# Performance work log

Hardware: AMD Instinct MI355X
Metric: run time of the kernel (lower is better)

## Reference

```python
import jax, jax.numpy as jnp
import numpy as np

EPS = 1e-5
SLOPE = 0.2
K = 20
B, N = 8, 2048

def _lrelu(x):
    return jnp.where(x >= 0, x, SLOPE * x)

def _bn(x, g, b, m, v, axis):
    # eval-mode batchnorm with running stats
    shape = [1] * x.ndim
    shape[axis] = -1
    g, b, m, v = (t.reshape(shape) for t in (g, b, m, v))
    return g * (x - m) * jax.lax.rsqrt(v + EPS) + b

def _knn(x, k):
    # x: (B, C, N) -> neighbor indices (B, N, k) by largest negative sq dist
    xx = jnp.sum(x * x, axis=1)                      # (B, N)
    inner = jnp.einsum('bcn,bcm->bnm', x, x)         # (B, N, N)
    pd = 2.0 * inner - xx[:, :, None] - xx[:, None, :]
    return jax.lax.top_k(pd, k)[1]

def _graph_feature(x, k):
    # x: (B, C, N) -> (B, 2C, N, k) edge features [nbr - center, center]
    idx = _knn(x, k)                                  # (B, N, k)
    xt = jnp.transpose(x, (0, 2, 1))                  # (B, N, C)
    nbr = xt[jnp.arange(x.shape[0])[:, None, None], idx]  # (B, N, k, C)
    center = xt[:, :, None, :]
    f = jnp.concatenate([nbr - center, jnp.broadcast_to(center, nbr.shape)], axis=-1)
    return jnp.transpose(f, (0, 3, 1, 2))

def _edge_block(x, W, g, b, m, v):
    f = _graph_feature(x, K)                          # (B, 2C, N, k)
    h = jnp.einsum('oc,bcnk->bonk', W, f)             # 1x1 conv
    return jnp.max(_lrelu(_bn(h, g, b, m, v, 1)), axis=-1)

def _forward(x, W1, bn1_g, bn1_b, bn1_m, bn1_v, W2, bn2_g, bn2_b, bn2_m, bn2_v, W3, bn3_g, bn3_b, bn3_m, bn3_v, W4, bn4_g, bn4_b, bn4_m, bn4_v, l1_w, l1_b, bn5_g, bn5_b, bn5_m, bn5_v, l2_w, l2_b, bn6_g, bn6_b, bn6_m, bn6_v, l3_w, l3_b):
    xc = jnp.transpose(x, (0, 2, 1))                  # (B, 3, N)
    x1 = _edge_block(xc, W1, bn1_g, bn1_b, bn1_m, bn1_v)   # (B, 64, N)
    x2 = _edge_block(x1, W2, bn2_g, bn2_b, bn2_m, bn2_v)   # (B, 64, N)
    x3 = _edge_block(x2, W3, bn3_g, bn3_b, bn3_m, bn3_v)   # (B, 128, N)
    h = jnp.concatenate([x1, x2, x3], axis=1)         # (B, 256, N)
    h = _lrelu(_bn(jnp.einsum('oc,bcn->bon', W4, h), bn4_g, bn4_b, bn4_m, bn4_v, 1))
    h = jnp.max(h, axis=-1)                           # (B, 1024)
    h = _lrelu(_bn(h @ l1_w.T + l1_b, bn5_g, bn5_b, bn5_m, bn5_v, 1))
    h = _lrelu(_bn(h @ l2_w.T + l2_b, bn6_g, bn6_b, bn6_m, bn6_v, 1))
    return h @ l3_w.T + l3_b                          # (B, 2)

def setup_inputs() -> dict:
    key = jax.random.key(0)
    ks = iter(jax.random.split(key, 64))
    def rn(shape, s=1.0):
        return jax.random.normal(next(ks), shape, jnp.float32) * s
    def add_bn(inp, prefix, c):
        inp[prefix + '_g'] = jax.random.uniform(next(ks), (c,), jnp.float32, 0.5, 1.5)
        inp[prefix + '_b'] = rn((c,), 0.1)
        inp[prefix + '_m'] = rn((c,), 0.1)
        inp[prefix + '_v'] = jax.random.uniform(next(ks), (c,), jnp.float32, 0.5, 1.5)
    inp = {'x': rn((B, N, 3))}
    inp['W1'] = rn((64, 6), 0.3); add_bn(inp, 'bn1', 64)
    inp['W2'] = rn((64, 128), 0.1); add_bn(inp, 'bn2', 64)
    inp['W3'] = rn((128, 128), 0.1); add_bn(inp, 'bn3', 128)
    inp['W4'] = rn((1024, 256), 0.08); add_bn(inp, 'bn4', 1024)
    inp['l1_w'] = rn((512, 1024), 0.03); inp['l1_b'] = rn((512,), 0.01); add_bn(inp, 'bn5', 512)
    inp['l2_w'] = rn((256, 512), 0.05); inp['l2_b'] = rn((256,), 0.01); add_bn(inp, 'bn6', 256)
    inp['l3_w'] = rn((2, 256), 0.06); inp['l3_b'] = rn((2,), 0.01)
    return inp

def reference(x, W1, bn1_g, bn1_b, bn1_m, bn1_v, W2, bn2_g, bn2_b, bn2_m, bn2_v, W3, bn3_g, bn3_b, bn3_m, bn3_v, W4, bn4_g, bn4_b, bn4_m, bn4_v, l1_w, l1_b, bn5_g, bn5_b, bn5_m, bn5_v, l2_w, l2_b, bn6_g, bn6_b, bn6_m, bn6_v, l3_w, l3_b):
    return _forward(x, W1, bn1_g, bn1_b, bn1_m, bn1_v, W2, bn2_g, bn2_b, bn2_m, bn2_v, W3, bn3_g, bn3_b, bn3_m, bn3_v, W4, bn4_g, bn4_b, bn4_m, bn4_v, l1_w, l1_b, bn5_g, bn5_b, bn5_m, bn5_v, l2_w, l2_b, bn6_g, bn6_b, bn6_m, bn6_v, l3_w, l3_b)
```

## Files before the change

kernel.cpp:

```cpp
#include <hip/hip_runtime.h>
#include <math.h>

#define BB 8
#define NN 2048
#define KK 20
#define EPSF 1e-5f
#define QB 32
#define NSP 8

__device__ __forceinline__ float lrelu(float v){ return v >= 0.f ? v : 0.2f*v; }

__device__ __forceinline__ void topk20_insert(float d, int idc, float (&v)[KK], int (&id)[KK]){
#pragma unroll
  for (int j = KK-1; j >= 1; --j){
    bool cjm1 = d > v[j-1];
    bool cj   = d > v[j];
    float nv = cjm1 ? v[j-1] : (cj ? d   : v[j]);
    int   ni = cjm1 ? id[j-1] : (cj ? idc : id[j]);
    v[j] = nv; id[j] = ni;
  }
  if (d > v[0]) { v[0] = d; id[0] = idc; }
}

__global__ void k_prep1(const float* __restrict__ x, const float* __restrict__ W1,
                        float* __restrict__ Y, float* __restrict__ T, float* __restrict__ SQ){
  __shared__ float wa[64][3], wd[64][3];
  int t = threadIdx.x;
  if (t < 64){
#pragma unroll
    for (int c=0;c<3;c++){
      float a = W1[t*6+c], b2 = W1[t*6+3+c];
      wa[t][c] = a; wd[t][c] = b2 - a;
    }
  }
  __syncthreads();
  int gid = blockIdx.x*256 + t;
  int b = gid >> 11, n = gid & (NN-1);
  float px = x[gid*3+0], py = x[gid*3+1], pz = x[gid*3+2];
  SQ[gid] = px*px + py*py + pz*pz;
  float* yb = Y + ((size_t)b*128)*NN + n;
  float* tb = T + ((size_t)b*128)*NN + n;
#pragma unroll 8
  for (int o=0;o<64;o++){
    yb[(size_t)o*NN] = wa[o][0]*px + wa[o][1]*py + wa[o][2]*pz;
    tb[(size_t)o*NN] = wd[o][0]*px + wd[o][1]*py + wd[o][2]*pz;
  }
}

__global__ __launch_bounds__(256) void k_knn3(const float* __restrict__ x, const float* __restrict__ SQ,
                                              int* __restrict__ IDX){
  __shared__ __align__(16) unsigned char smem[40960];
  float* cd = (float*)smem;
  float* VL = (float*)smem;
  int*   IL = (int*)(smem + 20480);
  int t = threadIdx.x;
  int b = blockIdx.x >> 6;
  int n_base = (blockIdx.x & 63) * QB;
  int ql = t & 31, sp = t >> 5;
  int n = n_base + ql;
  int gq = b*NN + n;
  float qx = x[gq*3], qy = x[gq*3+1], qz = x[gq*3+2];
  float qs = SQ[gq];
  float v[KK]; int id[KK];
#pragma unroll
  for (int i=0;i<KK;i++){ v[i] = -INFINITY; id[i] = 0; }
  int mlo = sp * 16;
  for (int tile=0; tile<16; ++tile){
    int m0 = tile * 128;
    __syncthreads();
#pragma unroll
    for (int i=0;i<2;i++){
      int f2 = t + i*256;
      int m = f2 >> 2, ch = f2 & 3;
      int gm = b*NN + m0 + m;
      cd[f2] = (ch < 3) ? x[gm*3 + ch] : SQ[gm];
    }
    __syncthreads();
    for (int j=mlo; j<mlo+16; ++j){
      float4 c4 = *(const float4*)&cd[j*4];
      float d = 2.f*(qx*c4.x + qy*c4.y + qz*c4.z) - qs - c4.w;
      if (d > v[KK-1]) topk20_insert(d, m0 + j, v, id);
    }
  }
  __syncthreads();
#pragma unroll
  for (int k2=0;k2<KK;k2++){
    VL[(ql*NSP+sp)*KK + k2] = v[k2];
    IL[(ql*NSP+sp)*KK + k2] = id[k2];
  }
  __syncthreads();
  if (t < QB){
    float hv[NSP]; int hi_[NSP]; int hp[NSP];
#pragma unroll
    for (int s=0;s<NSP;s++){ hp[s]=0; hv[s]=VL[(t*NSP+s)*KK]; hi_[s]=IL[(t*NSP+s)*KK]; }
    int nq = n_base + t;
    for (int r=0;r<KK;r++){
      float bv = hv[0]; int bi = hi_[0]; int bs = 0;
#pragma unroll
      for (int s=1;s<NSP;s++){
        bool win = (hv[s] > bv) || ((hv[s] == bv) && (hi_[s] < bi));
        bv = win ? hv[s] : bv; bi = win ? hi_[s] : bi; bs = win ? s : bs;
      }
      IDX[((size_t)b*KK + r)*NN + nq] = bi;
#pragma unroll
      for (int s=0;s<NSP;s++){
        if (s == bs){
          int np = hp[s] + 1; hp[s] = np;
          bool ok = np < KK;
          hv[s]  = ok ? VL[(t*NSP+s)*KK + np] : -INFINITY;
          hi_[s] = ok ? IL[(t*NSP+s)*KK + np] : 0x7FFFFFFF;
        }
      }
    }
  }
}

__global__ __launch_bounds__(256) void k_knn64(const float* __restrict__ X, const float* __restrict__ SQ,
                                               int* __restrict__ IDX){
  __shared__ __align__(16) unsigned char smem[40960];
  float* cd = (float*)smem;
  float* cs = (float*)(smem + 34816);
  float* VL = (float*)smem;
  int*   IL = (int*)(smem + 20480);
  int t = threadIdx.x;
  int b = blockIdx.x >> 6;
  int n_base = (blockIdx.x & 63) * QB;
  int ql = t & 31, sp = t >> 5;
  int n = n_base + ql;
  const float* xb = X + (size_t)b*256*NN;
  float q[64];
#pragma unroll
  for (int c=0;c<64;c++) q[c] = xb[(size_t)c*NN + n];
  float qs = SQ[b*NN + n];
  float v[KK]; int id[KK];
#pragma unroll
  for (int i=0;i<KK;i++){ v[i]=-INFINITY; id[i]=0; }
  int mlo = sp * 16;
  for (int tile=0; tile<16; ++tile){
    int m0 = tile*128;
    __syncthreads();
#pragma unroll
    for (int i=0;i<32;i++){
      int flat = i*256 + t;
      int c = flat >> 7, m = flat & 127;
      cd[m*68 + c] = xb[(size_t)c*NN + m0 + m];
    }
    if (t < 128) cs[t] = SQ[b*NN + m0 + t];
    __syncthreads();
    for (int j=mlo; j<mlo+16; ++j){
      float d = 0.f;
#pragma unroll
      for (int c=0;c<64;c+=4){
        float4 c4 = *(const float4*)&cd[j*68 + c];
        d += q[c]*c4.x + q[c+1]*c4.y + q[c+2]*c4.z + q[c+3]*c4.w;
      }
      d = 2.f*d - qs - cs[j];
      if (d > v[KK-1]) topk20_insert(d, m0 + j, v, id);
    }
  }
  __syncthreads();
#pragma unroll
  for (int k2=0;k2<KK;k2++){
    VL[(ql*NSP+sp)*KK + k2] = v[k2];
    IL[(ql*NSP+sp)*KK + k2] = id[k2];
  }
  __syncthreads();
  if (t < QB){
    float hv[NSP]; int hi_[NSP]; int hp[NSP];
#pragma unroll
    for (int s=0;s<NSP;s++){ hp[s]=0; hv[s]=VL[(t*NSP+s)*KK]; hi_[s]=IL[(t*NSP+s)*KK]; }
    int nq = n_base + t;
    for (int r=0;r<KK;r++){
      float bv = hv[0]; int bi = hi_[0]; int bs = 0;
#pragma unroll
      for (int s=1;s<NSP;s++){
        bool win = (hv[s] > bv) || ((hv[s] == bv) && (hi_[s] < bi));
        bv = win ? hv[s] : bv; bi = win ? hi_[s] : bi; bs = win ? s : bs;
      }
      IDX[((size_t)b*KK + r)*NN + nq] = bi;
#pragma unroll
      for (int s=0;s<NSP;s++){
        if (s == bs){
          int np = hp[s] + 1; hp[s] = np;
          bool ok = np < KK;
          hv[s]  = ok ? VL[(t*NSP+s)*KK + np] : -INFINITY;
          hi_[s] = ok ? IL[(t*NSP+s)*KK + np] : 0x7FFFFFFF;
        }
      }
    }
  }
}

__global__ void k_edge_apply(const float* __restrict__ Y, const float* __restrict__ T,
                             const int* __restrict__ IDX,
                             const float* __restrict__ g, const float* __restrict__ be,
                             const float* __restrict__ mu, const float* __restrict__ va,
                             float* __restrict__ OUT, int c_off){
  int n = blockIdx.x*256 + threadIdx.x;
  int o = blockIdx.y;
  int b = blockIdx.z;
  const float* yrow = Y + ((size_t)b*128 + o)*NN;
  float tval = T[((size_t)b*128 + o)*NN + n];
  float M = -INFINITY;
#pragma unroll
  for (int k2=0;k2<KK;k2++){
    int idn = IDX[((size_t)b*KK + k2)*NN + n];
    M = fmaxf(M, yrow[idn]);
  }
  float s = g[o] * rsqrtf(va[o] + EPSF);
  float val = s*(M + tval - mu[o]) + be[o];
  OUT[((size_t)b*256 + c_off + o)*NN + n] = lrelu(val);
}

__global__ void k_sqnorm(const float* __restrict__ X, float* __restrict__ SQ){
  int gid = blockIdx.x*256 + threadIdx.x;
  int b = gid >> 11, n = gid & (NN-1);
  const float* xb = X + (size_t)b*256*NN;
  float s = 0.f;
#pragma unroll
  for (int c=0;c<64;c++){ float vv = xb[(size_t)c*NN + n]; s += vv*vv; }
  SQ[gid] = s;
}

template<int O>
__global__ __launch_bounds__(256) void k_yt_gemm(const float* __restrict__ X, const float* __restrict__ W,
                                                 float* __restrict__ Y, float* __restrict__ T){
  __shared__ __align__(16) float wa[O][64];
  __shared__ __align__(16) float wd[O][64];
  int t = threadIdx.x;
  for (int i=t; i<O*64; i+=256){
    int o = i >> 6, c = i & 63;
    float a = W[o*128 + c];
    wa[o][c] = a;
    wd[o][c] = W[o*128 + 64 + c] - a;
  }
  __syncthreads();
  int half = t >> 7, ln = t & 127;
  int gid = blockIdx.x*128 + ln;
  int b = gid >> 11, n = gid & (NN-1);
  const float* xb = X + (size_t)b*256*NN;
  float q[64];
#pragma unroll
  for (int c=0;c<64;c++) q[c] = xb[(size_t)c*NN + n];
  int o0 = half * (O/2);
  for (int o=o0; o<o0+O/2; ++o){
    float ay=0.f, at=0.f;
#pragma unroll
    for (int c=0;c<64;c+=4){
      float4 a4 = *(const float4*)&wa[o][c];
      float4 d4 = *(const float4*)&wd[o][c];
      ay += a4.x*q[c] + a4.y*q[c+1] + a4.z*q[c+2] + a4.w*q[c+3];
      at += d4.x*q[c] + d4.y*q[c+1] + d4.z*q[c+2] + d4.w*q[c+3];
    }
    Y[((size_t)b*128 + o)*NN + n] = ay;
    T[((size_t)b*128 + o)*NN + n] = at;
  }
}

__global__ __launch_bounds__(256) void k_w4max(const float* __restrict__ CAT, const float* __restrict__ W4,
                                               float* __restrict__ PART){
  __shared__ __align__(16) float wt[64][68];
  __shared__ __align__(16) float ct[64][68];
  int t = threadIdx.x;
  int io = t >> 4, in_ = t & 15;
  int nb = blockIdx.x * 64, ob = blockIdx.y * 64, b = blockIdx.z;
  const float* catb = CAT + (size_t)b*256*NN;
  float acc[4][4];
#pragma unroll
  for (int r=0;r<4;r++)
#pragma unroll
    for (int c=0;c<4;c++) acc[r][c]=0.f;
  for (int c0=0; c0<256; c0+=64){
    __syncthreads();
    for (int i=t; i<4096; i+=256){
      int oo = i >> 6, cc = i & 63;
      wt[cc][oo] = W4[(size_t)(ob+oo)*256 + c0 + cc];
    }
    for (int i=t; i<4096; i+=256){
      int cc = i >> 6, nn2 = i & 63;
      ct[cc][nn2] = catb[(size_t)(c0+cc)*NN + nb + nn2];
    }
    __syncthreads();
#pragma unroll 4
    for (int c=0;c<64;c++){
      float4 wv = *(const float4*)&wt[c][io*4];
      float4 cv = *(const float4*)&ct[c][in_*4];
      acc[0][0] += wv.x*cv.x; acc[0][1] += wv.x*cv.y; acc[0][2] += wv.x*cv.z; acc[0][3] += wv.x*cv.w;
      acc[1][0] += wv.y*cv.x; acc[1][1] += wv.y*cv.y; acc[1][2] += wv.y*cv.z; acc[1][3] += wv.y*cv.w;
      acc[2][0] += wv.z*cv.x; acc[2][1] += wv.z*cv.y; acc[2][2] += wv.z*cv.z; acc[2][3] += wv.z*cv.w;
      acc[3][0] += wv.w*cv.x; acc[3][1] += wv.w*cv.y; acc[3][2] += wv.w*cv.z; acc[3][3] += wv.w*cv.w;
    }
  }
#pragma unroll
  for (int r=0;r<4;r++){
    float m = fmaxf(fmaxf(acc[r][0], acc[r][1]), fmaxf(acc[r][2], acc[r][3]));
    m = fmaxf(m, __shfl_xor(m, 1));
    m = fmaxf(m, __shfl_xor(m, 2));
    m = fmaxf(m, __shfl_xor(m, 4));
    m = fmaxf(m, __shfl_xor(m, 8));
    if (in_ == 0){
      int o = ob + io*4 + r;
      PART[((size_t)b*1024 + o)*32 + blockIdx.x] = m;
    }
  }
}

__global__ void k_reduce4(const float* __restrict__ PART,
                          const float* __restrict__ g, const float* __restrict__ be,
                          const float* __restrict__ mu, const float* __restrict__ va,
                          float* __restrict__ H4){
  int gid = blockIdx.x*256 + threadIdx.x;
  int o = gid & 1023;
  float M = -INFINITY;
#pragma unroll
  for (int i=0;i<32;i++) M = fmaxf(M, PART[(size_t)gid*32 + i]);
  float s = g[o]*rsqrtf(va[o]+EPSF);
  H4[gid] = lrelu(s*(M - mu[o]) + be[o]);
}

__global__ __launch_bounds__(256) void k_mlp(const float* __restrict__ H4,
      const float* __restrict__ l1w, const float* __restrict__ l1b,
      const float* __restrict__ g5, const float* __restrict__ b5,
      const float* __restrict__ m5, const float* __restrict__ v5,
      const float* __restrict__ l2w, const float* __restrict__ l2b,
      const float* __restrict__ g6, const float* __restrict__ b6,
      const float* __restrict__ m6, const float* __restrict__ v6,
      const float* __restrict__ l3w, const float* __restrict__ l3b,
      float* __restrict__ out){
  __shared__ float h[1024];
  __shared__ float h5[512];
  __shared__ float h6[256];
  int b = blockIdx.x, t = threadIdx.x;
  for (int i=t;i<1024;i+=256) h[i] = H4[b*1024+i];
  __syncthreads();
  for (int o=t;o<512;o+=256){
    float acc = l1b[o];
    for (int c=0;c<1024;c+=4){
      float4 w = *(const float4*)&l1w[(size_t)o*1024 + c];
      acc += w.x*h[c] + w.y*h[c+1] + w.z*h[c+2] + w.w*h[c+3];
    }
    float s = g5[o]*rsqrtf(v5[o]+EPSF);
    h5[o] = lrelu(s*(acc - m5[o]) + b5[o]);
  }
  __syncthreads();
  if (t < 256){
    int o = t;
    float acc = l2b[o];
    for (int c=0;c<512;c+=4){
      float4 w = *(const float4*)&l2w[(size_t)o*512 + c];
      acc += w.x*h5[c] + w.y*h5[c+1] + w.z*h5[c+2] + w.w*h5[c+3];
    }
    float s = g6[o]*rsqrtf(v6[o]+EPSF);
    h6[o] = lrelu(s*(acc - m6[o]) + b6[o]);
  }
  __syncthreads();
  if (t < 128){
    int o = t >> 6, l = t & 63;
    float p = 0.f;
#pragma unroll
    for (int j=0;j<4;j++){ int c = j*64 + l; p += l3w[o*256 + c]*h6[c]; }
    p += __shfl_xor(p, 32); p += __shfl_xor(p, 16); p += __shfl_xor(p, 8);
    p += __shfl_xor(p, 4);  p += __shfl_xor(p, 2);  p += __shfl_xor(p, 1);
    if (l == 0) out[b*2 + o] = p + l3b[o];
  }
}

extern "C" void kernel_launch(void* const* d_in, const int* in_sizes, int n_in,
                              void* d_out, int out_size, void* d_ws, size_t ws_size,
                              hipStream_t stream){
  (void)in_sizes; (void)n_in; (void)out_size; (void)ws_size;
  const float* x    = (const float*)d_in[0];
  const float* W1   = (const float*)d_in[1];
  const float* bn1g = (const float*)d_in[2];
  const float* bn1b = (const float*)d_in[3];
  const float* bn1m = (const float*)d_in[4];
  const float* bn1v = (const float*)d_in[5];
  const float* W2   = (const float*)d_in[6];
  const float* bn2g = (const float*)d_in[7];
  const float* bn2b = (const float*)d_in[8];
  const float* bn2m = (const float*)d_in[9];
  const float* bn2v = (const float*)d_in[10];
  const float* W3   = (const float*)d_in[11];
  const float* bn3g = (const float*)d_in[12];
  const float* bn3b = (const float*)d_in[13];
  const float* bn3m = (const float*)d_in[14];
  const float* bn3v = (const float*)d_in[15];
  const float* W4   = (const float*)d_in[16];
  const float* bn4g = (const float*)d_in[17];
  const float* bn4b = (const float*)d_in[18];
  const float* bn4m = (const float*)d_in[19];
  const float* bn4v = (const float*)d_in[20];
  const float* l1w  = (const float*)d_in[21];
  const float* l1b  = (const float*)d_in[22];
  const float* bn5g = (const float*)d_in[23];
  const float* bn5b = (const float*)d_in[24];
  const float* bn5m = (const float*)d_in[25];
  const float* bn5v = (const float*)d_in[26];
  const float* l2w  = (const float*)d_in[27];
  const float* l2b  = (const float*)d_in[28];
  const float* bn6g = (const float*)d_in[29];
  const float* bn6b = (const float*)d_in[30];
  const float* bn6m = (const float*)d_in[31];
  const float* bn6v = (const float*)d_in[32];
  const float* l3w  = (const float*)d_in[33];
  const float* l3b  = (const float*)d_in[34];

  float* CAT  = (float*)d_ws;
  float* Yb   = CAT + (size_t)8*256*2048;
  float* Tb   = Yb  + (size_t)8*128*2048;
  float* SQ   = Tb  + (size_t)8*128*2048;
  int*   IDX  = (int*)(SQ + (size_t)8*2048);
  float* PART = (float*)(IDX + (size_t)8*KK*2048);
  float* H4   = PART + (size_t)8*1024*32;

  k_prep1<<<64,256,0,stream>>>(x, W1, Yb, Tb, SQ);
  k_knn3<<<512,256,0,stream>>>(x, SQ, IDX);
  k_edge_apply<<<dim3(8,64,8),256,0,stream>>>(Yb, Tb, IDX, bn1g, bn1b, bn1m, bn1v, CAT, 0);
  k_sqnorm<<<64,256,0,stream>>>(CAT, SQ);
  k_knn64<<<512,256,0,stream>>>(CAT, SQ, IDX);
  k_yt_gemm<64><<<128,256,0,stream>>>(CAT, W2, Yb, Tb);
  k_edge_apply<<<dim3(8,64,8),256,0,stream>>>(Yb, Tb, IDX, bn2g, bn2b, bn2m, bn2v, CAT, 64);
  k_sqnorm<<<64,256,0,stream>>>(CAT + (size_t)64*2048, SQ);
  k_knn64<<<512,256,0,stream>>>(CAT + (size_t)64*2048, SQ, IDX);
  k_yt_gemm<128><<<128,256,0,stream>>>(CAT + (size_t)64*2048, W3, Yb, Tb);
  k_edge_apply<<<dim3(8,128,8),256,0,stream>>>(Yb, Tb, IDX, bn3g, bn3b, bn3m, bn3v, CAT, 128);
  k_w4max<<<dim3(32,16,8),256,0,stream>>>(CAT, W4, PART);
  k_reduce4<<<32,256,0,stream>>>(PART, bn4g, bn4b, bn4m, bn4v, H4);
  k_mlp<<<8,256,0,stream>>>(H4, l1w, l1b, bn5g, bn5b, bn5m, bn5v,
                            l2w, l2b, bn6g, bn6b, bn6m, bn6v, l3w, l3b, (float*)d_out);
}
```

Measured before the change: 1.509 ms.

## Split kNN queries across more threads, pre-transpose features, batch edge gather over channels

The kNN kernels now handle 16 queries per block with 16 candidate slices each, doubling the block count and halving each thread's serial top-k scan, at the cost of a larger 16-way merge. A new transpose kernel writes point-major 72-float rows with the squared norm packed in, which replaces the separate sqnorm kernel and lets kNN64 load queries and candidate tiles with float4 row copies. Edge-apply loads the 20 neighbour indices once per point and reuses them across 16 output channels. XT reuses the T buffer before the gemm rewrites it, so correctness depends on that ordering.

```diff
diff --git a/kernel.cpp b/kernel.cpp
--- a/kernel.cpp
+++ b/kernel.cpp
@@ -1,12 +1,9 @@
 #include <hip/hip_runtime.h>
 #include <math.h>
 
-#define BB 8
 #define NN 2048
 #define KK 20
 #define EPSF 1e-5f
-#define QB 32
-#define NSP 8
 
 __device__ __forceinline__ float lrelu(float v){ return v >= 0.f ? v : 0.2f*v; }
 
@@ -47,16 +44,16 @@
   }
 }
 
-__global__ __launch_bounds__(256) void k_knn3(const float* __restrict__ x, const float* __restrict__ SQ,
-                                              int* __restrict__ IDX){
+__global__ __launch_bounds__(256,4) void k_knn3(const float* __restrict__ x, const float* __restrict__ SQ,
+                                                int* __restrict__ IDX){
   __shared__ __align__(16) unsigned char smem[40960];
   float* cd = (float*)smem;
   float* VL = (float*)smem;
   int*   IL = (int*)(smem + 20480);
   int t = threadIdx.x;
-  int b = blockIdx.x >> 6;
-  int n_base = (blockIdx.x & 63) * QB;
-  int ql = t & 31, sp = t >> 5;
+  int b = blockIdx.x >> 7;
+  int n_base = (blockIdx.x & 127) * 16;
+  int ql = t & 15, sp = t >> 4;
   int n = n_base + ql;
   int gq = b*NN + n;
   float qx = x[gq*3], qy = x[gq*3+1], qz = x[gq*3+2];
@@ -64,7 +61,7 @@
   float v[KK]; int id[KK];
 #pragma unroll
   for (int i=0;i<KK;i++){ v[i] = -INFINITY; id[i] = 0; }
-  int mlo = sp * 16;
+  int mlo = sp * 8;
   for (int tile=0; tile<16; ++tile){
     int m0 = tile * 128;
     __syncthreads();
@@ -76,7 +73,7 @@
       cd[f2] = (ch < 3) ? x[gm*3 + ch] : SQ[gm];
     }
     __syncthreads();
-    for (int j=mlo; j<mlo+16; ++j){
+    for (int j=mlo; j<mlo+8; ++j){
       float4 c4 = *(const float4*)&cd[j*4];
       float d = 2.f*(qx*c4.x + qy*c4.y + qz*c4.z) - qs - c4.w;
       if (d > v[KK-1]) topk20_insert(d, m0 + j, v, id);
@@ -85,141 +82,173 @@
   __syncthreads();
 #pragma unroll
   for (int k2=0;k2<KK;k2++){
-    VL[(ql*NSP+sp)*KK + k2] = v[k2];
-    IL[(ql*NSP+sp)*KK + k2] = id[k2];
-  }
-  __syncthreads();
-  if (t < QB){
-    float hv[NSP]; int hi_[NSP]; int hp[NSP];
-#pragma unroll
-    for (int s=0;s<NSP;s++){ hp[s]=0; hv[s]=VL[(t*NSP+s)*KK]; hi_[s]=IL[(t*NSP+s)*KK]; }
+    VL[(ql*16+sp)*KK + k2] = v[k2];
+    IL[(ql*16+sp)*KK + k2] = id[k2];
+  }
+  __syncthreads();
+  if (t < 16){
+    float hv[16]; int hi_[16]; int hp[16];
+#pragma unroll
+    for (int s=0;s<16;s++){ hp[s]=0; hv[s]=VL[(t*16+s)*KK]; hi_[s]=IL[(t*16+s)*KK]; }
     int nq = n_base + t;
     for (int r=0;r<KK;r++){
       float bv = hv[0]; int bi = hi_[0]; int bs = 0;
 #pragma unroll
-      for (int s=1;s<NSP;s++){
+      for (int s=1;s<16;s++){
         bool win = (hv[s] > bv) || ((hv[s] == bv) && (hi_[s] < bi));
         bv = win ? hv[s] : bv; bi = win ? hi_[s] : bi; bs = win ? s : bs;
       }
       IDX[((size_t)b*KK + r)*NN + nq] = bi;
 #pragma unroll
-      for (int s=0;s<NSP;s++){
+      for (int s=0;s<16;s++){
         if (s == bs){
           int np = hp[s] + 1; hp[s] = np;
           bool ok = np < KK;
-          hv[s]  = ok ? VL[(t*NSP+s)*KK + np] : -INFINITY;
-          hi_[s] = ok ? IL[(t*NSP+s)*KK + np] : 0x7FFFFFFF;
+          hv[s]  = ok ? VL[(t*16+s)*KK + np] : -INFINITY;
+          hi_[s] = ok ? IL[(t*16+s)*KK + np] : 0x7FFFFFFF;
         }
       }
     }
   }
 }
 
-__global__ __launch_bounds__(256) void k_knn64(const float* __restrict__ X, const float* __restrict__ SQ,
-                                               int* __restrict__ IDX){
+__global__ __launch_bounds__(256) void k_transpose(const float* __restrict__ src, float* __restrict__ XT){
+  __shared__ float Tt[64][65];
+  int t = threadIdx.x;
+  int b = blockIdx.y;
+  int n0 = blockIdx.x * 64;
+  const float* sb = src + (size_t)b*256*NN;
+#pragma unroll
+  for (int i=0;i<16;i++){
+    int flat = i*256 + t;
+    int c = flat >> 6, n = flat & 63;
+    Tt[c][n] = sb[(size_t)c*NN + n0 + n];
+  }
+  __syncthreads();
+  float sqv = 0.f;
+  if (t < 64){
+#pragma unroll
+    for (int c=0;c<64;c++){ float vv = Tt[c][t]; sqv += vv*vv; }
+  }
+  float* orow = XT + ((size_t)b*NN + n0)*72;
+#pragma unroll
+  for (int i=0;i<16;i++){
+    int flat = i*256 + t;
+    int n = flat >> 6, c = flat & 63;
+    orow[(size_t)n*72 + c] = Tt[c][n];
+  }
+  if (t < 64){
+    orow[(size_t)t*72 + 64] = sqv;
+#pragma unroll
+    for (int p=65;p<72;p++) orow[(size_t)t*72 + p] = 0.f;
+  }
+}
+
+__global__ __launch_bounds__(256,4) void k_knn64(const float* __restrict__ XT, int* __restrict__ IDX){
   __shared__ __align__(16) unsigned char smem[40960];
   float* cd = (float*)smem;
-  float* cs = (float*)(smem + 34816);
   float* VL = (float*)smem;
   int*   IL = (int*)(smem + 20480);
   int t = threadIdx.x;
-  int b = blockIdx.x >> 6;
-  int n_base = (blockIdx.x & 63) * QB;
-  int ql = t & 31, sp = t >> 5;
+  int b = blockIdx.x >> 7;
+  int n_base = (blockIdx.x & 127) * 16;
+  int ql = t & 15, sp = t >> 4;
   int n = n_base + ql;
-  const float* xb = X + (size_t)b*256*NN;
+  const float* qrow = XT + ((size_t)b*NN + n)*72;
   float q[64];
 #pragma unroll
-  for (int c=0;c<64;c++) q[c] = xb[(size_t)c*NN + n];
-  float qs = SQ[b*NN + n];
+  for (int c=0;c<64;c+=4){
+    float4 qv = *(const float4*)(qrow + c);
+    q[c]=qv.x; q[c+1]=qv.y; q[c+2]=qv.z; q[c+3]=qv.w;
+  }
+  float qs = qrow[64];
   float v[KK]; int id[KK];
 #pragma unroll
   for (int i=0;i<KK;i++){ v[i]=-INFINITY; id[i]=0; }
-  int mlo = sp * 16;
+  int mlo = sp * 8;
+  int mrow = t >> 1, mh = t & 1;
   for (int tile=0; tile<16; ++tile){
     int m0 = tile*128;
     __syncthreads();
-#pragma unroll
-    for (int i=0;i<32;i++){
-      int flat = i*256 + t;
-      int c = flat >> 7, m = flat & 127;
-      cd[m*68 + c] = xb[(size_t)c*NN + m0 + m];
-    }
-    if (t < 128) cs[t] = SQ[b*NN + m0 + t];
-    __syncthreads();
-    for (int j=mlo; j<mlo+16; ++j){
+    const float* srow = XT + ((size_t)b*NN + m0 + mrow)*72;
+    float* drow = cd + mrow*68;
+#pragma unroll
+    for (int i=0;i<9;i++){
+      int k = mh*9 + i;
+      if (k < 17){
+        float4 vv4 = *(const float4*)(srow + 4*k);
+        *(float4*)(drow + 4*k) = vv4;
+      }
+    }
+    __syncthreads();
+    for (int j=mlo; j<mlo+8; ++j){
+      const float* crow = cd + j*68;
       float d = 0.f;
 #pragma unroll
       for (int c=0;c<64;c+=4){
-        float4 c4 = *(const float4*)&cd[j*68 + c];
+        float4 c4 = *(const float4*)(crow + c);
         d += q[c]*c4.x + q[c+1]*c4.y + q[c+2]*c4.z + q[c+3]*c4.w;
       }
-      d = 2.f*d - qs - cs[j];
+      d = 2.f*d - qs - crow[64];
       if (d > v[KK-1]) topk20_insert(d, m0 + j, v, id);
     }
   }
   __syncthreads();
 #pragma unroll
   for (int k2=0;k2<KK;k2++){
-    VL[(ql*NSP+sp)*KK + k2] = v[k2];
-    IL[(ql*NSP+sp)*KK + k2] = id[k2];
-  }
-  __syncthreads();
-  if (t < QB){
-    float hv[NSP]; int hi_[NSP]; int hp[NSP];
-#pragma unroll
-    for (int s=0;s<NSP;s++){ hp[s]=0; hv[s]=VL[(t*NSP+s)*KK]; hi_[s]=IL[(t*NSP+s)*KK]; }
+    VL[(ql*16+sp)*KK + k2] = v[k2];
+    IL[(ql*16+sp)*KK + k2] = id[k2];
+  }
+  __syncthreads();
+  if (t < 16){
+    float hv[16]; int hi_[16]; int hp[16];
+#pragma unroll
+    for (int s=0;s<16;s++){ hp[s]=0; hv[s]=VL[(t*16+s)*KK]; hi_[s]=IL[(t*16+s)*KK]; }
     int nq = n_base + t;
     for (int r=0;r<KK;r++){
       float bv = hv[0]; int bi = hi_[0]; int bs = 0;
 #pragma unroll
-      for (int s=1;s<NSP;s++){
+      for (int s=1;s<16;s++){
         bool win = (hv[s] > bv) || ((hv[s] == bv) && (hi_[s] < bi));
         bv = win ? hv[s] : bv; bi = win ? hi_[s] : bi; bs = win ? s : bs;
       }
       IDX[((size_t)b*KK + r)*NN + nq] = bi;
 #pragma unroll
-      for (int s=0;s<NSP;s++){
+      for (int s=0;s<16;s++){
         if (s == bs){
           int np = hp[s] + 1; hp[s] = np;
           bool ok = np < KK;
-          hv[s]  = ok ? VL[(t*NSP+s)*KK + np] : -INFINITY;
-          hi_[s] = ok ? IL[(t*NSP+s)*KK + np] : 0x7FFFFFFF;
+          hv[s]  = ok ? VL[(t*16+s)*KK + np] : -INFINITY;
+          hi_[s] = ok ? IL[(t*16+s)*KK + np] : 0x7FFFFFFF;
         }
       }
     }
   }
 }
 
-__global__ void k_edge_apply(const float* __restrict__ Y, const float* __restrict__ T,
+__global__ __launch_bounds__(256) void k_edge_apply(const float* __restrict__ Y, const float* __restrict__ T,
                              const int* __restrict__ IDX,
                              const float* __restrict__ g, const float* __restrict__ be,
                              const float* __restrict__ mu, const float* __restrict__ va,
                              float* __restrict__ OUT, int c_off){
-  int n = blockIdx.x*256 + threadIdx.x;
-  int o = blockIdx.y;
+  int t = threadIdx.x;
+  int nl = t & 127, oh = t >> 7;
+  int n = blockIdx.x*128 + nl;
   int b = blockIdx.z;
-  const float* yrow = Y + ((size_t)b*128 + o)*NN;
-  float tval = T[((size_t)b*128 + o)*NN + n];
-  float M = -INFINITY;
-#pragma unroll
-  for (int k2=0;k2<KK;k2++){
-    int idn = IDX[((size_t)b*KK + k2)*NN + n];
-    M = fmaxf(M, yrow[idn]);
-  }
-  float s = g[o] * rsqrtf(va[o] + EPSF);
-  float val = s*(M + tval - mu[o]) + be[o];
-  OUT[((size_t)b*256 + c_off + o)*NN + n] = lrelu(val);
-}
-
-__global__ void k_sqnorm(const float* __restrict__ X, float* __restrict__ SQ){
-  int gid = blockIdx.x*256 + threadIdx.x;
-  int b = gid >> 11, n = gid & (NN-1);
-  const float* xb = X + (size_t)b*256*NN;
-  float s = 0.f;
-#pragma unroll
-  for (int c=0;c<64;c++){ float vv = xb[(size_t)c*NN + n]; s += vv*vv; }
-  SQ[gid] = s;
+  int o0 = blockIdx.y*32 + oh*16;
+  int idx[KK];
+#pragma unroll
+  for (int k2=0;k2<KK;k2++) idx[k2] = IDX[((size_t)b*KK + k2)*NN + n];
+  for (int oo=0;oo<16;oo++){
+    int o = o0 + oo;
+    const float* yrow = Y + ((size_t)b*128 + o)*NN;
+    float M = -INFINITY;
+#pragma unroll
+    for (int k2=0;k2<KK;k2++) M = fmaxf(M, yrow[idx[k2]]);
+    float s = g[o] * rsqrtf(va[o] + EPSF);
+    float val = s*(M + T[((size_t)b*128 + o)*NN + n] - mu[o]) + be[o];
+    OUT[((size_t)b*256 + c_off + o)*NN + n] = lrelu(val);
+  }
 }
 
 template<int O>
@@ -406,24 +435,25 @@
   const float* l3b  = (const float*)d_in[34];
 
   float* CAT  = (float*)d_ws;
-  float* Yb   = CAT + (size_t)8*256*2048;
-  float* Tb   = Yb  + (size_t)8*128*2048;
-  float* SQ   = Tb  + (size_t)8*128*2048;
-  int*   IDX  = (int*)(SQ + (size_t)8*2048);
-  float* PART = (float*)(IDX + (size_t)8*KK*2048);
+  float* Yb   = CAT + (size_t)8*256*NN;
+  float* Tb   = Yb  + (size_t)8*128*NN;
+  float* SQ   = Tb  + (size_t)8*128*NN;
+  int*   IDX  = (int*)(SQ + (size_t)8*NN);
+  float* PART = (float*)(IDX + (size_t)8*KK*NN);
   float* H4   = PART + (size_t)8*1024*32;
+  float* XT   = Tb;
 
   k_prep1<<<64,256,0,stream>>>(x, W1, Yb, Tb, SQ);
-  k_knn3<<<512,256,0,stream>>>(x, SQ, IDX);
-  k_edge_apply<<<dim3(8,64,8),256,0,stream>>>(Yb, Tb, IDX, bn1g, bn1b, bn1m, bn1v, CAT, 0);
-  k_sqnorm<<<64,256,0,stream>>>(CAT, SQ);
-  k_knn64<<<512,256,0,stream>>>(CAT, SQ, IDX);
+  k_knn3<<<1024,256,0,stream>>>(x, SQ, IDX);
+  k_edge_apply<<<dim3(16,2,8),256,0,stream>>>(Yb, Tb, IDX, bn1g, bn1b, bn1m, bn1v, CAT, 0);
+  k_transpose<<<dim3(32,8),256,0,stream>>>(CAT, XT);
+  k_knn64<<<1024,256,0,stream>>>(XT, IDX);
   k_yt_gemm<64><<<128,256,0,stream>>>(CAT, W2, Yb, Tb);
-  k_edge_apply<<<dim3(8,64,8),256,0,stream>>>(Yb, Tb, IDX, bn2g, bn2b, bn2m, bn2v, CAT, 64);
-  k_sqnorm<<<64,256,0,stream>>>(CAT + (size_t)64*2048, SQ);
-  k_knn64<<<512,256,0,stream>>>(CAT + (size_t)64*2048, SQ, IDX);
-  k_yt_gemm<128><<<128,256,0,stream>>>(CAT + (size_t)64*2048, W3, Yb, Tb);
-  k_edge_apply<<<dim3(8,128,8),256,0,stream>>>(Yb, Tb, IDX, bn3g, bn3b, bn3m, bn3v, CAT, 128);
+  k_edge_apply<<<dim3(16,2,8),256,0,stream>>>(Yb, Tb, IDX, bn2g, bn2b, bn2m, bn2v, CAT, 64);
+  k_transpose<<<dim3(32,8),256,0,stream>>>(CAT + (size_t)64*NN, XT);
+  k_knn64<<<1024,256,0,stream>>>(XT, IDX);
+  k_yt_gemm<128><<<128,256,0,stream>>>(CAT + (size_t)64*NN, W3, Yb, Tb);
+  k_edge_apply<<<dim3(16,4,8),256,0,stream>>>(Yb, Tb, IDX, bn3g, bn3b, bn3m, bn3v, CAT, 128);
   k_w4max<<<dim3(32,16,8),256,0,stream>>>(CAT, W4, PART);
   k_reduce4<<<32,256,0,stream>>>(PART, bn4g, bn4b, bn4m, bn4v, H4);
   k_mlp<<<8,256,0,stream>>>(H4, l1w, l1b, bn5g, bn5b, bn5m, bn5v,
```

Result: slower. 1.973 ms (+30.8%).
